# Kernel optimization log

Hardware: AMD Instinct MI355X
Metric: run time of the kernel (lower is better)

## Reference

```python
import math
import jax, jax.numpy as jnp
import numpy as np

RS_IN = [(128, 0), (64, 1), (32, 2)]
RS_OUT = [(128, 0), (64, 1), (32, 2)]
SET_LF = [0, 1, 2, 3, 4]
BATCH = 512
HIDDEN = 64

def _lfilters(l_in, l_out):
    return list(range(abs(l_in - l_out), l_in + l_out + 1))

N_PATH = sum(mo * mi * len(_lfilters(li, lo)) for mo, lo in RS_OUT for mi, li in RS_IN)  # 70656

# ---------- Clebsch-Gordan (numpy, setup time only) ----------

def _su2_cg(j1, j2, j3):
    f = math.factorial
    C = np.zeros((2 * j1 + 1, 2 * j2 + 1, 2 * j3 + 1))
    for m1 in range(-j1, j1 + 1):
        for m2 in range(-j2, j2 + 1):
            m3 = m1 + m2
            if abs(m3) > j3:
                continue
            pref = math.sqrt((2 * j3 + 1) * f(j3 + j1 - j2) * f(j3 - j1 + j2) * f(j1 + j2 - j3) / f(j1 + j2 + j3 + 1))
            pref *= math.sqrt(f(j3 + m3) * f(j3 - m3) * f(j1 - m1) * f(j1 + m1) * f(j2 - m2) * f(j2 + m2))
            s = 0.0
            for v in range(0, j1 + j2 - j3 + 1):
                d = [v, j1 + j2 - j3 - v, j1 - m1 - v, j2 + m2 - v, j3 - j2 + m1 + v, j3 - j1 - m2 + v]
                if any(x < 0 for x in d):
                    continue
                s += (-1) ** v / float(np.prod([f(x) for x in d]))
            C[j1 + m1, j2 + m2, j3 + m3] = pref * s
    return C

def _r2c(l):
    # change of basis real -> complex spherical harmonics, with phase making CG real
    q = np.zeros((2 * l + 1, 2 * l + 1), dtype=complex)
    for m in range(-l, 0):
        q[l + m, l + abs(m)] = 1 / math.sqrt(2)
        q[l + m, l - abs(m)] = -1j / math.sqrt(2)
    q[l, l] = 1
    for m in range(1, l + 1):
        q[l + m, l + abs(m)] = (-1) ** m / math.sqrt(2)
        q[l + m, l - abs(m)] = 1j * (-1) ** m / math.sqrt(2)
    return ((-1j) ** l) * q

def _cg_real(l1, l2, l3):
    C = np.einsum('ai,bj,ck,abc->ijk', _r2c(l1), _r2c(l2), np.conj(_r2c(l3)), _su2_cg(l1, l2, l3))
    C = C.imag if np.abs(C.imag).sum() > np.abs(C.real).sum() else C.real
    n = np.linalg.norm(C)
    return C / n if n > 0 else C

# ---------- real spherical harmonics (jax) ----------

def _sh(ls, r):
    # r: [batch, 3] -> Y: [sum(2l+1 for l in ls), batch]
    eps = 1e-9
    nrm = jnp.linalg.norm(r, axis=1, keepdims=True)
    d = r / jnp.maximum(nrm, eps)
    x, y, z = d[:, 0], d[:, 1], d[:, 2]
    rxy = jnp.sqrt(jnp.maximum(x * x + y * y, eps * eps))
    cphi, sphi = x / rxy, y / rxy
    lmax = max(ls)
    somx2 = jnp.sqrt(jnp.maximum(1.0 - z * z, 1e-12))
    P = {}
    pmm = jnp.ones_like(z)
    for m in range(lmax + 1):
        if m > 0:
            pmm = pmm * (2 * m - 1) * somx2
        P[(m, m)] = pmm
        if m + 1 <= lmax:
            P[(m + 1, m)] = z * (2 * m + 1) * pmm
        for l in range(m + 2, lmax + 1):
            P[(l, m)] = ((2 * l - 1) * z * P[(l - 1, m)] - (l + m - 1) * P[(l - 2, m)]) / (l - m)
    cm = [jnp.ones_like(z), cphi]
    sm = [jnp.zeros_like(z), sphi]
    for m in range(2, lmax + 1):
        cm.append(cm[m - 1] * cphi - sm[m - 1] * sphi)
        sm.append(sm[m - 1] * cphi + cm[m - 1] * sphi)
    f = math.factorial
    rows = []
    for l in ls:
        for m in range(-l, l + 1):
            am = abs(m)
            N = math.sqrt((2 * l + 1) / (4 * math.pi) * f(l - am) / f(l + am))
            if m == 0:
                rows.append(N * P[(l, 0)])
            elif m > 0:
                rows.append(math.sqrt(2) * N * P[(l, am)] * cm[am])
            else:
                rows.append(math.sqrt(2) * N * P[(l, am)] * sm[am])
    return jnp.stack(rows, axis=0)

# ---------- kernel forward ----------

def _kernel_forward(r, w1, b1, w2, b2, Qs):
    batch = r.shape[0]
    Ys = _sh(SET_LF, r)                       # [25, batch]
    radii = jnp.linalg.norm(r, axis=1)        # [batch]
    h = jax.nn.relu(radii[:, None] @ w1 + b1) # [batch, HIDDEN]
    coefficients = h @ w2 + b2                # [batch, N_PATH]
    begin_c = 0
    out_blocks = []
    for i, (mul_out, l_out) in enumerate(RS_OUT):
        num_summed = sum(mul_in * len(_lfilters(l_in, l_out)) for mul_in, l_in in RS_IN)
        in_blocks = []
        for j, (mul_in, l_in) in enumerate(RS_IN):
            lfs = _lfilters(l_in, l_out)
            n = mul_out * mul_in * len(lfs)
            c = coefficients[:, begin_c:begin_c + n].reshape(batch, mul_out, mul_in, len(lfs))
            begin_c += n
            Qij = Qs[i][j]
            K = 0
            for k, lf in enumerate(lfs):
                off_y = sum(2 * l + 1 for l in SET_LF if l < lf)
                Y = Ys[off_y:off_y + 2 * lf + 1]                 # [2lf+1, batch]
                off_q = sum(2 * l + 1 for l in lfs if l < lf)
                Q = Qij[:, :, off_q:off_q + 2 * lf + 1]          # [2lo+1, 2li+1, 2lf+1]
                K = K + jnp.einsum('ijk,kz,zuv->zuivj', Q, Y, c[..., k])
            # normalization == 'norm'
            xnorm = math.sqrt(2 * l_in + 1) * math.sqrt(4 * math.pi) / math.sqrt(num_summed)
            K = K * xnorm
            in_blocks.append(K.reshape(batch, mul_out * (2 * l_out + 1), mul_in * (2 * l_in + 1)))
        out_blocks.append(jnp.concatenate(in_blocks, axis=2))
    return jnp.concatenate(out_blocks, axis=1)  # [batch, 480, 480]

def setup_inputs() -> dict:
    key = jax.random.key(0)
    ks = jax.random.split(key, 5)
    inp = {}
    inp['r'] = jax.random.normal(ks[0], (BATCH, 3), dtype=jnp.float32)
    inp['w1'] = jax.random.normal(ks[1], (1, HIDDEN), dtype=jnp.float32) * 0.5
    inp['b1'] = jax.random.normal(ks[2], (HIDDEN,), dtype=jnp.float32) * 0.1
    inp['w2'] = jax.random.normal(ks[3], (HIDDEN, N_PATH), dtype=jnp.float32) * (1.0 / math.sqrt(HIDDEN))
    inp['b2'] = jax.random.normal(ks[4], (N_PATH,), dtype=jnp.float32) * 0.01
    for i, (mo, lo) in enumerate(RS_OUT):
        for j, (mi, li) in enumerate(RS_IN):
            Q = np.concatenate([_cg_real(lo, li, lf) for lf in _lfilters(li, lo)], axis=2)
            inp['Q_%d_%d' % (i, j)] = jnp.asarray(Q, dtype=jnp.float32)
    return inp

def reference(r, w1, b1, w2, b2, Q_0_0, Q_0_1, Q_0_2, Q_1_0, Q_1_1, Q_1_2, Q_2_0, Q_2_1, Q_2_2):
    Qs = [[Q_0_0, Q_0_1, Q_0_2], [Q_1_0, Q_1_1, Q_1_2], [Q_2_0, Q_2_1, Q_2_2]]
    return _kernel_forward(r, w1, b1, w2, b2, Qs)
```

## Files before the change

kernel.cpp:

```cpp
#include <hip/hip_runtime.h>
#include <math.h>

#define NPATH 70656
#define NBATCH 512
#define OUTD 480
#define OUTSZ (OUTD*OUTD)
#define ZCHV_S 32
#define ZCHV_T 32
#define ZTS 8
#define ZTT 8

constexpr int CBEG_TAB[9] = {0,16384,24576,28672,36864,49152,55296,59392,65536};

struct QPtrs { const float* q[9]; };

__global__ __launch_bounds__(256) void sh_mlp_kernel(
    const float* __restrict__ r, const float* __restrict__ w1,
    const float* __restrict__ b1, float* __restrict__ Yg,
    float* __restrict__ hTz)
{
  int z = blockIdx.x*256 + threadIdx.x;
  if (z >= NBATCH) return;
  float x = r[3*z], y = r[3*z+1], zz = r[3*z+2];
  float nrm = sqrtf(x*x + y*y + zz*zz);
  float inv = 1.0f / fmaxf(nrm, 1e-9f);
  float dx = x*inv, dy = y*inv, dz = zz*inv;
  float rxy = sqrtf(fmaxf(dx*dx + dy*dy, 1e-18f));
  float cphi = dx/rxy, sphi = dy/rxy;
  float somx2 = sqrtf(fmaxf(1.0f - dz*dz, 1e-12f));

  float P[5][5];
  float pmm = 1.0f;
  #pragma unroll
  for (int m = 0; m < 5; ++m) {
    if (m > 0) pmm *= (float)(2*m-1) * somx2;
    P[m][m] = pmm;
    if (m+1 < 5) P[m+1][m] = dz * (float)(2*m+1) * pmm;
    #pragma unroll
    for (int l = m+2; l < 5; ++l)
      P[l][m] = ((float)(2*l-1)*dz*P[l-1][m] - (float)(l+m-1)*P[l-2][m]) / (float)(l-m);
  }
  float cm[5], sm[5];
  cm[0]=1.0f; sm[0]=0.0f; cm[1]=cphi; sm[1]=sphi;
  #pragma unroll
  for (int m = 2; m < 5; ++m) {
    cm[m] = cm[m-1]*cphi - sm[m-1]*sphi;
    sm[m] = sm[m-1]*cphi + cm[m-1]*sphi;
  }
  const float fact[9] = {1,1,2,6,24,120,720,5040,40320};
  int row = 0;
  #pragma unroll
  for (int l = 0; l < 5; ++l) {
    #pragma unroll
    for (int m = -l; m <= l; ++m) {
      int am = m < 0 ? -m : m;
      float N = sqrtf((float)(2*l+1) / 12.566370614359172f * fact[l-am] / fact[l+am]);
      float v;
      if (m == 0)      v = N * P[l][0];
      else if (m > 0)  v = 1.4142135623730951f * N * P[l][am] * cm[am];
      else             v = 1.4142135623730951f * N * P[l][am] * sm[am];
      Yg[z*25 + row] = v;
      ++row;
    }
  }
  #pragma unroll
  for (int k = 0; k < 64; ++k)
    hTz[z*64 + k] = fmaxf(nrm * w1[k] + b1[k], 0.0f);
}

template<int LO, int LI>
__device__ __forceinline__ void stream_body(
    int bidl, const float* __restrict__ Yg, const float* __restrict__ hTz,
    const float* __restrict__ w2f, const float* __restrict__ b2,
    const float* __restrict__ Q, float* __restrict__ out,
    float* h_lds, float* Y_lds)
{
  constexpr int DI = 2*LO+1, DJ = 2*LI+1;
  constexpr int MI = 128>>LI;
  constexpr int NUV = (128>>LO)*MI;
  constexpr int UVB = NUV/256;
  constexpr int LF = LO+LI;
  constexpr int MAXM = 2*LF+1;
  constexpr int ROWOFF = (LO==0)?0:((LO==1)?128:320);
  constexpr int COLOFF = (LI==0)?0:((LI==1)?128:320);
  constexpr int CBEG = CBEG_TAB[LO*3+LI];
  constexpr float NS = (LO==0)?224.0f:((LO==1)?416.0f:480.0f);
  const float xn = sqrtf((float)(2*LI+1) * 12.566370614359172f / NS);

  const int tid = threadIdx.x;
  const int uvb   = bidl % UVB;
  const int chunk = bidl / UVB;
  const int z0 = chunk * ZCHV_S;
  const int uv = uvb*256 + tid;
  const int uu = uv >> (7-LI);
  const int vv = uv & (MI-1);
  const int path = CBEG + uv;
  const float b2p = b2[path];

  #pragma unroll
  for (int i = tid; i < ZCHV_S*16; i += 256)
    ((float4*)h_lds)[i] = ((const float4*)(hTz + (size_t)z0*64))[i];
  for (int i = tid; i < ZCHV_S*25; i += 256)
    Y_lds[i] = Yg[(size_t)z0*25 + i];
  __syncthreads();

  float Qv[DI*DJ][MAXM];
  #pragma unroll
  for (int ij = 0; ij < DI*DJ; ++ij)
    #pragma unroll
    for (int m = 0; m < MAXM; ++m)
      Qv[ij][m] = Q[ij*MAXM + m];

  float* outR = out + (size_t)(ROWOFF + uu*DI)*OUTD + COLOFF + vv*DJ;

  for (int t0 = 0; t0 < ZCHV_S; t0 += ZTS) {
    float acc[ZTS];
    #pragma unroll
    for (int zt = 0; zt < ZTS; ++zt) acc[zt] = b2p;
    #pragma unroll
    for (int kk = 0; kk < 64; kk += 16) {
      float w2c[16];
      #pragma unroll
      for (int k = 0; k < 16; ++k)
        w2c[k] = w2f[(size_t)(kk+k)*NPATH + path];
      #pragma unroll
      for (int zt = 0; zt < ZTS; ++zt) {
        const float* hz = h_lds + (t0+zt)*64 + kk;
        float h[16];
        #pragma unroll
        for (int q = 0; q < 16; q += 4) *(float4*)&h[q] = *(const float4*)(hz+q);
        float s0=0.f, s1=0.f, s2=0.f, s3=0.f;
        #pragma unroll
        for (int k = 0; k < 16; k += 4) {
          s0 = fmaf(h[k],   w2c[k],   s0);
          s1 = fmaf(h[k+1], w2c[k+1], s1);
          s2 = fmaf(h[k+2], w2c[k+2], s2);
          s3 = fmaf(h[k+3], w2c[k+3], s3);
        }
        acc[zt] += (s0+s1)+(s2+s3);
      }
    }
    #pragma unroll
    for (int zt = 0; zt < ZTS; ++zt) {
      const int zl = t0 + zt;
      const float* yz = Y_lds + zl*25 + LF*LF;
      const float c = acc[zt]*xn;
      float* oz = outR + (size_t)(z0+zl)*OUTSZ;
      #pragma unroll
      for (int i = 0; i < DI; ++i)
        #pragma unroll
        for (int j = 0; j < DJ; ++j) {
          float a = 0.0f;
          #pragma unroll
          for (int m = 0; m < MAXM; ++m) a = fmaf(Qv[i*DJ+j][m], yz[m], a);
          oz[i*OUTD + j] = a*c;
        }
    }
  }
}

template<int LO, int LI>
__device__ __forceinline__ void tiled_body(
    int bidl, const float* __restrict__ Yg, const float* __restrict__ hTz,
    const float* __restrict__ w2f, const float* __restrict__ b2,
    const float* __restrict__ Q, float* __restrict__ out,
    float* c_lds, float* A_lds, float* h_lds)
{
  constexpr int DI = 2*LO+1, DJ = 2*LI+1;
  constexpr int MO = 128>>LO, MI = 128>>LI;
  constexpr int NL = 2*((LO<LI)?LO:LI)+1;
  constexpr int LF0 = (LO>LI)?(LO-LI):(LI-LO);
  constexpr int QDIM = (LO+LI+1)*(LO+LI+1) - LF0*LF0;
  constexpr int NUV = MO*MI;
  constexpr int G = 256/NL;
  constexpr int UVB = (NUV + G - 1)/G;
  constexpr int NOUT = G*DI*DJ;
  constexpr int OPT = (NOUT + 255)/256;
  constexpr int ASIZE = DI*DJ*NL;
  constexpr int MAXM = 2*(LO+LI)+1;
  constexpr int ROWOFF = (LO==0)?0:((LO==1)?128:320);
  constexpr int COLOFF = (LI==0)?0:((LI==1)?128:320);
  constexpr int CBEG = CBEG_TAB[LO*3+LI];
  constexpr float NS = (LO==0)?224.0f:((LO==1)?416.0f:480.0f);
  const float xn = sqrtf((float)(2*LI+1) * 12.566370614359172f / NS);

  const int tid = threadIdx.x;
  const int uvb   = bidl % UVB;
  const int chunk = bidl / UVB;
  const int uv0 = uvb * G;
  const int z0  = chunk * ZCHV_T;

  const int gl = tid / NL;
  const int kf = tid % NL;
  const bool cact = (gl < G) && (uv0 + gl < NUV);
  const int path = CBEG + (cact ? ((uv0+gl)*NL + kf) : 0);
  const float b2p = b2[path];

  #pragma unroll
  for (int i = tid; i < ZCHV_T*16; i += 256)
    ((float4*)h_lds)[i] = ((const float4*)(hTz + (size_t)z0*64))[i];

  float Qv[MAXM];
  int yb = 0;
  {
    int t = (tid < ASIZE) ? tid : 0;
    int i  = t / (DJ*NL);
    int j  = (t / NL) % DJ;
    int kA = t % NL;
    int lf = LF0 + kA;
    int qoff = kA*(2*LF0 + kA);
    int mlim = 2*lf + 1;
    yb = lf*lf;
    #pragma unroll
    for (int m = 0; m < MAXM; ++m)
      Qv[m] = (m < mlim) ? Q[(i*DJ + j)*QDIM + qoff + m] : 0.0f;
  }

  int rowoff_o[OPT], aidx_o[OPT], cidx_o[OPT];
  bool val_o[OPT];
  #pragma unroll
  for (int t = 0; t < OPT; ++t) {
    int o = tid + 256*t;
    bool v = o < NOUT;
    int oo = v ? o : 0;
    int i   = oo / (G*DJ);
    int rem = oo % (G*DJ);
    int g   = rem / DJ;
    int j   = rem % DJ;
    int uv  = uv0 + g;
    v = v && (uv < NUV);
    int uu = uv >> (7-LI);
    int vv = uv & (MI-1);
    rowoff_o[t] = (uu*DI + i)*OUTD + vv*DJ + j;
    aidx_o[t] = (i*DJ + j)*NL;
    cidx_o[t] = g*NL;
    val_o[t] = v;
  }
  __syncthreads();

  float* outR = out + ROWOFF*OUTD + COLOFF;

  for (int tile = 0; tile < ZCHV_T/ZTT; ++tile) {
    const int p = tile & 1;
    float* cb = c_lds + p*(ZTT*256);
    float* ab = A_lds + p*(ZTT*128);
    const int zb = z0 + tile*ZTT;

    float acc[ZTT];
    #pragma unroll
    for (int zt = 0; zt < ZTT; ++zt) acc[zt] = b2p;
    #pragma unroll
    for (int kk = 0; kk < 64; kk += 16) {
      float w2c[16];
      #pragma unroll
      for (int k = 0; k < 16; ++k)
        w2c[k] = w2f[(size_t)(kk+k)*NPATH + path];
      #pragma unroll
      for (int zt = 0; zt < ZTT; ++zt) {
        const float* hz = h_lds + (tile*ZTT+zt)*64 + kk;
        float h[16];
        #pragma unroll
        for (int q = 0; q < 16; q += 4) *(float4*)&h[q] = *(const float4*)(hz+q);
        float s0=0.f, s1=0.f, s2=0.f, s3=0.f;
        #pragma unroll
        for (int k = 0; k < 16; k += 4) {
          s0 = fmaf(h[k],   w2c[k],   s0);
          s1 = fmaf(h[k+1], w2c[k+1], s1);
          s2 = fmaf(h[k+2], w2c[k+2], s2);
          s3 = fmaf(h[k+3], w2c[k+3], s3);
        }
        acc[zt] += (s0+s1)+(s2+s3);
      }
    }
    #pragma unroll
    for (int zt = 0; zt < ZTT; ++zt) cb[zt*256 + tid] = acc[zt];

    if (tid < ASIZE) {
      #pragma unroll
      for (int zt = 0; zt < ZTT; ++zt) {
        const float* yz = Yg + (size_t)(zb+zt)*25 + yb;
        float s = 0.0f;
        #pragma unroll
        for (int m = 0; m < MAXM; ++m) s = fmaf(Qv[m], yz[m], s);
        ab[zt*128 + tid] = s;
      }
    }
    asm volatile("s_waitcnt lgkmcnt(0)\n\ts_barrier" ::: "memory");

    for (int zt = 0; zt < ZTT; ++zt) {
      float* oz = outR + (size_t)(zb+zt)*OUTSZ;
      const float* cbz = cb + zt*256;
      const float* abz = ab + zt*128;
      #pragma unroll
      for (int t = 0; t < OPT; ++t) {
        if (val_o[t]) {
          float s = 0.0f;
          #pragma unroll
          for (int k = 0; k < NL; ++k) s += abz[aidx_o[t] + k] * cbz[cidx_o[t] + k];
          oz[rowoff_o[t]] = s*xn;
        }
      }
    }
  }
}

__global__ __launch_bounds__(256) void tp_stream_kernel(
    const float* __restrict__ Yg, const float* __restrict__ hTz,
    const float* __restrict__ w2, const float* __restrict__ b2,
    QPtrs qp, float* __restrict__ out)
{
  __shared__ float h_lds[ZCHV_S*64];
  __shared__ float Y_lds[ZCHV_S*25];
  const int b = blockIdx.x;
  const int chunk = b / 160;
  const int r = b % 160;
  if      (r <  64) stream_body<0,0>(chunk*64 + r,      Yg,hTz,w2,b2,qp.q[0],out,h_lds,Y_lds);
  else if (r <  96) stream_body<0,1>(chunk*32 + (r- 64),Yg,hTz,w2,b2,qp.q[1],out,h_lds,Y_lds);
  else if (r < 112) stream_body<0,2>(chunk*16 + (r- 96),Yg,hTz,w2,b2,qp.q[2],out,h_lds,Y_lds);
  else if (r < 144) stream_body<1,0>(chunk*32 + (r-112),Yg,hTz,w2,b2,qp.q[3],out,h_lds,Y_lds);
  else              stream_body<2,0>(chunk*16 + (r-144),Yg,hTz,w2,b2,qp.q[6],out,h_lds,Y_lds);
}

__global__ __launch_bounds__(256) void tp_tiled_kernel(
    const float* __restrict__ Yg, const float* __restrict__ hTz,
    const float* __restrict__ w2, const float* __restrict__ b2,
    QPtrs qp, float* __restrict__ out)
{
  __shared__ float c_lds[2*ZTT*256];
  __shared__ float A_lds[2*ZTT*128];
  __shared__ float h_lds[ZCHV_T*64];
  const int b = blockIdx.x;
  const int chunk = b / 120;
  const int r = b % 120;
  if      (r <  49) tiled_body<1,1>(chunk*49 + r,      Yg,hTz,w2,b2,qp.q[4],out,c_lds,A_lds,h_lds);
  else if (r <  74) tiled_body<1,2>(chunk*25 + (r-49), Yg,hTz,w2,b2,qp.q[5],out,c_lds,A_lds,h_lds);
  else if (r <  99) tiled_body<2,1>(chunk*25 + (r-74), Yg,hTz,w2,b2,qp.q[7],out,c_lds,A_lds,h_lds);
  else              tiled_body<2,2>(chunk*21 + (r-99), Yg,hTz,w2,b2,qp.q[8],out,c_lds,A_lds,h_lds);
}

extern "C" void kernel_launch(void* const* d_in, const int* in_sizes, int n_in,
                              void* d_out, int out_size, void* d_ws, size_t ws_size,
                              hipStream_t stream)
{
  (void)in_sizes; (void)n_in; (void)out_size; (void)ws_size;
  const float* r  = (const float*)d_in[0];
  const float* w1 = (const float*)d_in[1];
  const float* b1 = (const float*)d_in[2];
  const float* w2 = (const float*)d_in[3];
  const float* b2 = (const float*)d_in[4];
  float* out = (float*)d_out;

  float* ws  = (float*)d_ws;
  float* Yg  = ws;
  float* hTz = ws + 12800;

  QPtrs qp;
  for (int i = 0; i < 9; ++i) qp.q[i] = (const float*)d_in[5 + i];

  hipLaunchKernelGGL(sh_mlp_kernel, dim3(2), dim3(256), 0, stream, r, w1, b1, Yg, hTz);
  hipLaunchKernelGGL(tp_tiled_kernel,  dim3((NBATCH/ZCHV_T)*120), dim3(256), 0, stream,
                     Yg, hTz, w2, b2, qp, out);
  hipLaunchKernelGGL(tp_stream_kernel, dim3((NBATCH/ZCHV_S)*160), dim3(256), 0, stream,
                     Yg, hTz, w2, b2, qp, out);
}
```

Baseline: 191.7 us.

## Merge stream and tiled tensor-product kernels into one launch with shared LDS

Combines the two tensor-product kernels into a single launch, dispatching stream and tiled block bodies by block index within each batch chunk. The LDS is unified into one 20KB buffer: h_lds is shared by both paths, and Y_lds aliases c_lds. The tiled path's double-buffered c/A LDS is replaced with single buffers guarded by an extra barrier at the start of each tile. The aim is to remove a kernel launch boundary and let heavy and light blocks overlap on the GPU, in exchange for an added barrier per tile and a different LDS footprint that may change occupancy.

Result: slower. 222.4 us (+16.0%).

```diff
diff --git a/kernel.cpp b/kernel.cpp
--- a/kernel.cpp
+++ b/kernel.cpp
@@ -5,8 +5,7 @@
 #define NBATCH 512
 #define OUTD 480
 #define OUTSZ (OUTD*OUTD)
-#define ZCHV_S 32
-#define ZCHV_T 32
+#define ZCHV 32
 #define ZTS 8
 #define ZTT 8
 
@@ -90,7 +89,7 @@
   const int tid = threadIdx.x;
   const int uvb   = bidl % UVB;
   const int chunk = bidl / UVB;
-  const int z0 = chunk * ZCHV_S;
+  const int z0 = chunk * ZCHV;
   const int uv = uvb*256 + tid;
   const int uu = uv >> (7-LI);
   const int vv = uv & (MI-1);
@@ -98,9 +97,9 @@
   const float b2p = b2[path];
 
   #pragma unroll
-  for (int i = tid; i < ZCHV_S*16; i += 256)
+  for (int i = tid; i < ZCHV*16; i += 256)
     ((float4*)h_lds)[i] = ((const float4*)(hTz + (size_t)z0*64))[i];
-  for (int i = tid; i < ZCHV_S*25; i += 256)
+  for (int i = tid; i < ZCHV*25; i += 256)
     Y_lds[i] = Yg[(size_t)z0*25 + i];
   __syncthreads();
 
@@ -113,7 +112,7 @@
 
   float* outR = out + (size_t)(ROWOFF + uu*DI)*OUTD + COLOFF + vv*DJ;
 
-  for (int t0 = 0; t0 < ZCHV_S; t0 += ZTS) {
+  for (int t0 = 0; t0 < ZCHV; t0 += ZTS) {
     float acc[ZTS];
     #pragma unroll
     for (int zt = 0; zt < ZTS; ++zt) acc[zt] = b2p;
@@ -188,7 +187,7 @@
   const int uvb   = bidl % UVB;
   const int chunk = bidl / UVB;
   const int uv0 = uvb * G;
-  const int z0  = chunk * ZCHV_T;
+  const int z0  = chunk * ZCHV;
 
   const int gl = tid / NL;
   const int kf = tid % NL;
@@ -197,7 +196,7 @@
   const float b2p = b2[path];
 
   #pragma unroll
-  for (int i = tid; i < ZCHV_T*16; i += 256)
+  for (int i = tid; i < ZCHV*16; i += 256)
     ((float4*)h_lds)[i] = ((const float4*)(hTz + (size_t)z0*64))[i];
 
   float Qv[MAXM];
@@ -240,11 +239,11 @@
 
   float* outR = out + ROWOFF*OUTD + COLOFF;
 
-  for (int tile = 0; tile < ZCHV_T/ZTT; ++tile) {
-    const int p = tile & 1;
-    float* cb = c_lds + p*(ZTT*256);
-    float* ab = A_lds + p*(ZTT*128);
+  for (int tile = 0; tile < ZCHV/ZTT; ++tile) {
     const int zb = z0 + tile*ZTT;
+
+    if (tile > 0)
+      asm volatile("s_waitcnt lgkmcnt(0)\n\ts_barrier" ::: "memory");
 
     float acc[ZTT];
     #pragma unroll
@@ -273,7 +272,7 @@
       }
     }
     #pragma unroll
-    for (int zt = 0; zt < ZTT; ++zt) cb[zt*256 + tid] = acc[zt];
+    for (int zt = 0; zt < ZTT; ++zt) c_lds[zt*256 + tid] = acc[zt];
 
     if (tid < ASIZE) {
       #pragma unroll
@@ -282,15 +281,15 @@
         float s = 0.0f;
         #pragma unroll
         for (int m = 0; m < MAXM; ++m) s = fmaf(Qv[m], yz[m], s);
-        ab[zt*128 + tid] = s;
+        A_lds[zt*128 + tid] = s;
       }
     }
     asm volatile("s_waitcnt lgkmcnt(0)\n\ts_barrier" ::: "memory");
 
     for (int zt = 0; zt < ZTT; ++zt) {
       float* oz = outR + (size_t)(zb+zt)*OUTSZ;
-      const float* cbz = cb + zt*256;
-      const float* abz = ab + zt*128;
+      const float* cbz = c_lds + zt*256;
+      const float* abz = A_lds + zt*128;
       #pragma unroll
       for (int t = 0; t < OPT; ++t) {
         if (val_o[t]) {
@@ -304,38 +303,28 @@
   }
 }
 
-__global__ __launch_bounds__(256) void tp_stream_kernel(
+__global__ __launch_bounds__(256) void tp_kernel(
     const float* __restrict__ Yg, const float* __restrict__ hTz,
     const float* __restrict__ w2, const float* __restrict__ b2,
     QPtrs qp, float* __restrict__ out)
 {
-  __shared__ float h_lds[ZCHV_S*64];
-  __shared__ float Y_lds[ZCHV_S*25];
+  __shared__ float lds[5120];
+  float* h_lds = lds;
+  float* Y_lds = lds + 2048;
+  float* c_lds = lds + 2048;
+  float* A_lds = lds + 4096;
   const int b = blockIdx.x;
-  const int chunk = b / 160;
-  const int r = b % 160;
+  const int chunk = b / 280;
+  const int r = b % 280;
   if      (r <  64) stream_body<0,0>(chunk*64 + r,      Yg,hTz,w2,b2,qp.q[0],out,h_lds,Y_lds);
   else if (r <  96) stream_body<0,1>(chunk*32 + (r- 64),Yg,hTz,w2,b2,qp.q[1],out,h_lds,Y_lds);
   else if (r < 112) stream_body<0,2>(chunk*16 + (r- 96),Yg,hTz,w2,b2,qp.q[2],out,h_lds,Y_lds);
   else if (r < 144) stream_body<1,0>(chunk*32 + (r-112),Yg,hTz,w2,b2,qp.q[3],out,h_lds,Y_lds);
-  else              stream_body<2,0>(chunk*16 + (r-144),Yg,hTz,w2,b2,qp.q[6],out,h_lds,Y_lds);
-}
-
-__global__ __launch_bounds__(256) void tp_tiled_kernel(
-    const float* __restrict__ Yg, const float* __restrict__ hTz,
-    const float* __restrict__ w2, const float* __restrict__ b2,
-    QPtrs qp, float* __restrict__ out)
-{
-  __shared__ float c_lds[2*ZTT*256];
-  __shared__ float A_lds[2*ZTT*128];
-  __shared__ float h_lds[ZCHV_T*64];
-  const int b = blockIdx.x;
-  const int chunk = b / 120;
-  const int r = b % 120;
-  if      (r <  49) tiled_body<1,1>(chunk*49 + r,      Yg,hTz,w2,b2,qp.q[4],out,c_lds,A_lds,h_lds);
-  else if (r <  74) tiled_body<1,2>(chunk*25 + (r-49), Yg,hTz,w2,b2,qp.q[5],out,c_lds,A_lds,h_lds);
-  else if (r <  99) tiled_body<2,1>(chunk*25 + (r-74), Yg,hTz,w2,b2,qp.q[7],out,c_lds,A_lds,h_lds);
-  else              tiled_body<2,2>(chunk*21 + (r-99), Yg,hTz,w2,b2,qp.q[8],out,c_lds,A_lds,h_lds);
+  else if (r < 160) stream_body<2,0>(chunk*16 + (r-144),Yg,hTz,w2,b2,qp.q[6],out,h_lds,Y_lds);
+  else if (r < 209) tiled_body<1,1>(chunk*49 + (r-160), Yg,hTz,w2,b2,qp.q[4],out,c_lds,A_lds,h_lds);
+  else if (r < 234) tiled_body<1,2>(chunk*25 + (r-209), Yg,hTz,w2,b2,qp.q[5],out,c_lds,A_lds,h_lds);
+  else if (r < 259) tiled_body<2,1>(chunk*25 + (r-234), Yg,hTz,w2,b2,qp.q[7],out,c_lds,A_lds,h_lds);
+  else              tiled_body<2,2>(chunk*21 + (r-259), Yg,hTz,w2,b2,qp.q[8],out,c_lds,A_lds,h_lds);
 }
 
 extern "C" void kernel_launch(void* const* d_in, const int* in_sizes, int n_in,
@@ -358,8 +347,6 @@
   for (int i = 0; i < 9; ++i) qp.q[i] = (const float*)d_in[5 + i];
 
   hipLaunchKernelGGL(sh_mlp_kernel, dim3(2), dim3(256), 0, stream, r, w1, b1, Yg, hTz);
-  hipLaunchKernelGGL(tp_tiled_kernel,  dim3((NBATCH/ZCHV_T)*120), dim3(256), 0, stream,
+  hipLaunchKernelGGL(tp_kernel, dim3((NBATCH/ZCHV)*280), dim3(256), 0, stream,
                      Yg, hTz, w2, b2, qp, out);
-  hipLaunchKernelGGL(tp_stream_kernel, dim3((NBATCH/ZCHV_S)*160), dim3(256), 0, stream,
-                     Yg, hTz, w2, b2, qp, out);
-}
+}
```

## Restructure tiled output stage to per-(g,i) rows with vectorized LDS reads

Applied to the files above, without the earlier changes.

Each thread now handles one (uv-group, output row i) pair and writes a full row of DJ contiguous outputs. Coefficients and A values are read from LDS as padded float4 vectors instead of scalar reads per output. The c/A LDS buffers go from double-buffered to single-buffered, which adds a barrier at the start of each tile. The aim is fewer LDS loads and less per-output index bookkeeping, at the cost of an extra barrier and fewer active threads for small pair counts.

Result: no change. 194.6 us (+1.5%).

```diff
diff --git a/kernel.cpp b/kernel.cpp
--- a/kernel.cpp
+++ b/kernel.cpp
@@ -174,10 +174,12 @@
   constexpr int NUV = MO*MI;
   constexpr int G = 256/NL;
   constexpr int UVB = (NUV + G - 1)/G;
-  constexpr int NOUT = G*DI*DJ;
-  constexpr int OPT = (NOUT + 255)/256;
   constexpr int ASIZE = DI*DJ*NL;
   constexpr int MAXM = 2*(LO+LI)+1;
+  constexpr int CP   = (NL==3)?4:8;
+  constexpr int AROW = ((DJ*NL + 3)/4)*4;
+  constexpr int NPAIR = G*DI;
+  constexpr int PPT  = (NPAIR + 255)/256;
   constexpr int ROWOFF = (LO==0)?0:((LO==1)?128:320);
   constexpr int COLOFF = (LI==0)?0:((LI==1)?128:320);
   constexpr int CBEG = CBEG_TAB[LO*3+LI];
@@ -201,50 +203,47 @@
     ((float4*)h_lds)[i] = ((const float4*)(hTz + (size_t)z0*64))[i];
 
   float Qv[MAXM];
-  int yb = 0;
+  int yb = 0, aoff = 0;
   {
     int t = (tid < ASIZE) ? tid : 0;
-    int i  = t / (DJ*NL);
-    int j  = (t / NL) % DJ;
-    int kA = t % NL;
+    int i   = t / (DJ*NL);
+    int rem = t % (DJ*NL);
+    int kA  = rem % NL;
     int lf = LF0 + kA;
     int qoff = kA*(2*LF0 + kA);
     int mlim = 2*lf + 1;
     yb = lf*lf;
+    aoff = i*AROW + rem;
     #pragma unroll
     for (int m = 0; m < MAXM; ++m)
-      Qv[m] = (m < mlim) ? Q[(i*DJ + j)*QDIM + qoff + m] : 0.0f;
-  }
-
-  int rowoff_o[OPT], aidx_o[OPT], cidx_o[OPT];
-  bool val_o[OPT];
-  #pragma unroll
-  for (int t = 0; t < OPT; ++t) {
-    int o = tid + 256*t;
-    bool v = o < NOUT;
-    int oo = v ? o : 0;
-    int i   = oo / (G*DJ);
-    int rem = oo % (G*DJ);
-    int g   = rem / DJ;
-    int j   = rem % DJ;
-    int uv  = uv0 + g;
+      Qv[m] = (m < mlim) ? Q[(t/(DJ*NL)*DJ + (rem/NL))*QDIM + qoff + m] : 0.0f;
+  }
+
+  int g_o[PPT], i_o[PPT], ooff_o[PPT];
+  bool val_o[PPT];
+  #pragma unroll
+  for (int pp = 0; pp < PPT; ++pp) {
+    int p = tid + 256*pp;
+    bool v = p < NPAIR;
+    int pc = v ? p : 0;
+    int g = pc % G, i = pc / G;
+    int uv = uv0 + g;
     v = v && (uv < NUV);
     int uu = uv >> (7-LI);
     int vv = uv & (MI-1);
-    rowoff_o[t] = (uu*DI + i)*OUTD + vv*DJ + j;
-    aidx_o[t] = (i*DJ + j)*NL;
-    cidx_o[t] = g*NL;
-    val_o[t] = v;
+    g_o[pp] = g; i_o[pp] = i;
+    ooff_o[pp] = (uu*DI + i)*OUTD + vv*DJ;
+    val_o[pp] = v;
   }
   __syncthreads();
 
   float* outR = out + ROWOFF*OUTD + COLOFF;
 
   for (int tile = 0; tile < ZCHV_T/ZTT; ++tile) {
-    const int p = tile & 1;
-    float* cb = c_lds + p*(ZTT*256);
-    float* ab = A_lds + p*(ZTT*128);
     const int zb = z0 + tile*ZTT;
+
+    if (tile > 0)
+      asm volatile("s_waitcnt lgkmcnt(0)\n\ts_barrier" ::: "memory");
 
     float acc[ZTT];
     #pragma unroll
@@ -272,8 +271,10 @@
         acc[zt] += (s0+s1)+(s2+s3);
       }
     }
-    #pragma unroll
-    for (int zt = 0; zt < ZTT; ++zt) cb[zt*256 + tid] = acc[zt];
+    if (gl < G) {
+      #pragma unroll
+      for (int zt = 0; zt < ZTT; ++zt) c_lds[zt*(G*CP) + gl*CP + kf] = acc[zt];
+    }
 
     if (tid < ASIZE) {
       #pragma unroll
@@ -282,22 +283,34 @@
         float s = 0.0f;
         #pragma unroll
         for (int m = 0; m < MAXM; ++m) s = fmaf(Qv[m], yz[m], s);
-        ab[zt*128 + tid] = s;
+        A_lds[zt*(DI*AROW) + aoff] = s;
       }
     }
     asm volatile("s_waitcnt lgkmcnt(0)\n\ts_barrier" ::: "memory");
 
     for (int zt = 0; zt < ZTT; ++zt) {
       float* oz = outR + (size_t)(zb+zt)*OUTSZ;
-      const float* cbz = cb + zt*256;
-      const float* abz = ab + zt*128;
-      #pragma unroll
-      for (int t = 0; t < OPT; ++t) {
-        if (val_o[t]) {
-          float s = 0.0f;
+      const float* cbz = c_lds + zt*(G*CP);
+      const float* abz = A_lds + zt*(DI*AROW);
+      #pragma unroll
+      for (int pp = 0; pp < PPT; ++pp) {
+        if (val_o[pp]) {
+          float cvf[CP];
           #pragma unroll
-          for (int k = 0; k < NL; ++k) s += abz[aidx_o[t] + k] * cbz[cidx_o[t] + k];
-          oz[rowoff_o[t]] = s*xn;
+          for (int q = 0; q < CP; q += 4)
+            *(float4*)&cvf[q] = *(const float4*)(cbz + g_o[pp]*CP + q);
+          float avf[AROW];
+          #pragma unroll
+          for (int q = 0; q < AROW; q += 4)
+            *(float4*)&avf[q] = *(const float4*)(abz + i_o[pp]*AROW + q);
+          float* op = oz + ooff_o[pp];
+          #pragma unroll
+          for (int j = 0; j < DJ; ++j) {
+            float s = 0.0f;
+            #pragma unroll
+            for (int k = 0; k < NL; ++k) s = fmaf(avf[j*NL + k], cvf[k], s);
+            op[j] = s*xn;
+          }
         }
       }
     }
@@ -326,9 +339,9 @@
     const float* __restrict__ w2, const float* __restrict__ b2,
     QPtrs qp, float* __restrict__ out)
 {
-  __shared__ float c_lds[2*ZTT*256];
-  __shared__ float A_lds[2*ZTT*128];
-  __shared__ float h_lds[ZCHV_T*64];
+  __shared__ __align__(16) float c_lds[3264];
+  __shared__ __align__(16) float A_lds[1120];
+  __shared__ __align__(16) float h_lds[ZCHV_T*64];
   const int b = blockIdx.x;
   const int chunk = b / 120;
   const int r = b % 120;
```
